# Optimization experiments

Hardware: AMD Instinct MI355X
Metric: run time of the kernel (lower is better)

## Reference

```python
import jax, jax.numpy as jnp
import numpy as np


def conv1x1(x, w, b):
    # x: [B,C,H,W], w: [O,C], b: [O]
    return jnp.einsum('bchw,oc->bohw', x, w) + b[None, :, None, None]


def dwconv(x, w):
    # depthwise conv, x: [B,C,H,W], w: [C,1,k,k], SAME padding (k odd, pad=k//2)
    return jax.lax.conv_general_dilated(
        x, w, window_strides=(1, 1), padding='SAME',
        dimension_numbers=('NCHW', 'OIHW', 'NCHW'),
        feature_group_count=x.shape[1])


def setup_inputs() -> dict:
    key = jax.random.key(0)
    ks = jax.random.split(key, 14)
    B, C, H, W = 16, 256, 64, 64
    OC = C // 16  # scale=16 -> 16
    WSCALE = 0.05
    r = lambda k, shape: jax.random.normal(k, shape, dtype=jnp.float32) * WSCALE
    return {
        'x': jax.random.normal(ks[0], (B, C, H, W), dtype=jnp.float32),
        'conv_w': r(ks[1], (C + 4, C)),           # 1x1 conv -> ctx (C) + gates (3+1)
        'conv_b': r(ks[2], (C + 4,)),
        'fw3': r(ks[3], (C, 1, 3, 3)),            # depthwise focal kernels
        'fw5': r(ks[4], (C, 1, 5, 5)),
        'fw7': r(ks[5], (C, 1, 7, 7)),
        'key_w': r(ks[6], (1, C)),                # Conv_key 1x1
        'key_b': r(ks[7], (1,)),
        'v1_w': r(ks[8], (OC, C)),                # Conv_value first 1x1
        'v1_b': r(ks[9], (OC,)),
        'ln_w': jnp.ones((OC,), dtype=jnp.float32),
        'ln_b': jnp.zeros((OC,), dtype=jnp.float32),
        'v2_w': r(ks[10], (C, OC)),               # Conv_value second 1x1
        'v2_b': r(ks[11], (C,)),
    }


def reference(x, conv_w, conv_b, fw3, fw5, fw7, key_w, key_b,
              v1_w, v1_b, ln_w, ln_b, v2_w, v2_b):
    B, C, H, W = x.shape
    # _contextAggregation
    t = conv1x1(x, conv_w, conv_b)          # [B, C+4, H, W]
    ctx, gates = t[:, :C], t[:, C:]         # [B,C,H,W], [B,4,H,W]
    ctx_all = jnp.zeros_like(ctx)
    for l, fw in enumerate((fw3, fw5, fw7)):
        ctx = jax.nn.gelu(dwconv(ctx, fw), approximate=False)  # torch GELU = exact erf
        ctx_all = ctx_all + ctx * gates[:, l:l + 1]
    ctx_global = jnp.mean(ctx, axis=(2, 3), keepdims=True)     # AdaptiveAvgPool2d(1)
    ctx_all = ctx_all + ctx_global * gates[:, 3:4]
    # GC-style channel attention: softmax over spatial positions
    k = conv1x1(ctx_all, key_w, key_b).reshape(B, H * W)       # [B, HW]
    k = jax.nn.softmax(k, axis=1)
    q = ctx_all.reshape(B, C, H * W)
    qk = jnp.einsum('bcn,bn->bc', q, k)[:, :, None, None]      # [B,C,1,1]
    # Conv_value: 1x1 -> LayerNorm([OC,1,1]) -> ReLU -> 1x1
    v = conv1x1(qk, v1_w, v1_b)                                # [B,OC,1,1]
    mu = jnp.mean(v, axis=(1, 2, 3), keepdims=True)
    var = jnp.var(v, axis=(1, 2, 3), keepdims=True)
    v = (v - mu) * jax.lax.rsqrt(var + 1e-5)
    v = v * ln_w[None, :, None, None] + ln_b[None, :, None, None]
    v = jax.nn.relu(v)
    v = conv1x1(v, v2_w, v2_b)                                 # [B,C,1,1]
    return ctx_all + v
```

## Files before the change

### kernel.cpp

```cpp
#include <hip/hip_runtime.h>

#define DEVFN __device__ __forceinline__

constexpr int B  = 16;
constexpr int C  = 256;
constexpr int N  = 64 * 64;
constexpr int O1 = C + 4;

typedef __attribute__((ext_vector_type(8)))  short bf16x8;
typedef __attribute__((ext_vector_type(4)))  short bf16x4;
typedef __attribute__((ext_vector_type(16))) float f32x16;
typedef unsigned short ushort_t;

DEVFN short f2bf(float f){
  union { float f; unsigned u; } p; p.f = f;
  unsigned r = p.u + 0x7fffu + ((p.u >> 16) & 1u);
  return (short)(r >> 16);
}
DEVFN float lo2f(unsigned u){ union{unsigned u; float f;} p; p.u = u << 16; return p.f; }
DEVFN float hi2f(unsigned u){ union{unsigned u; float f;} p; p.u = u & 0xffff0000u; return p.f; }

DEVFN float gelu_fast(float x){
  float y = 1.5957691216f * fmaf(0.044715f * x * x, x, x);
  return x / (1.0f + __expf(-y));
}

__global__ __launch_bounds__(256, 4)
void k_conv1_mfma(const float* __restrict__ x, const float* __restrict__ w,
                  const float* __restrict__ bias, ushort_t* __restrict__ ctxb,
                  float* __restrict__ gates){
  __shared__ __align__(16) short wlds[16 * 64 * 8];
  __shared__ __align__(16) short xlds[16 * 64 * 8];
  const int tid  = threadIdx.x;
  const int wv   = tid >> 6;
  const int lane = tid & 63;
  const int l31  = lane & 31;
  const int lhi  = lane >> 5;
  const int oBase = blockIdx.y * 64;
  const int pg0   = blockIdx.x * 64;
  const int b  = pg0 >> 12;
  const int n0 = pg0 & 4095;
  const int mw = (wv >> 1) * 32;
  const int nw = (wv & 1) * 32;

  f32x16 acc;
  #pragma unroll
  for(int r = 0; r < 16; r++) acc[r] = 0.f;

  const int rstage = tid & 63;
  const int kg0    = (tid >> 6) * 4;

  for(int kc = 0; kc < 256; kc += 128){
    __syncthreads();
    {
      const int o = oBase + rstage;
      const float* wp = w + o * 256 + kc;
      #pragma unroll
      for(int t = 0; t < 4; t++){
        const int kg = kg0 + t;
        bf16x8 v;
        if(o < O1){
          const float4 f0 = *(const float4*)(wp + kg * 8);
          const float4 f1 = *(const float4*)(wp + kg * 8 + 4);
          v[0] = f2bf(f0.x); v[1] = f2bf(f0.y); v[2] = f2bf(f0.z); v[3] = f2bf(f0.w);
          v[4] = f2bf(f1.x); v[5] = f2bf(f1.y); v[6] = f2bf(f1.z); v[7] = f2bf(f1.w);
        } else {
          #pragma unroll
          for(int j = 0; j < 8; j++) v[j] = 0;
        }
        *(bf16x8*)&wlds[(kg * 64 + rstage) * 8] = v;
      }
    }
    {
      const float* xp = x + (size_t)b * C * N + (size_t)kc * N + n0 + rstage;
      #pragma unroll
      for(int t = 0; t < 4; t++){
        const int kg = kg0 + t;
        float f[8];
        #pragma unroll
        for(int j = 0; j < 8; j++) f[j] = xp[(size_t)(kg * 8 + j) * N];
        bf16x8 v;
        #pragma unroll
        for(int j = 0; j < 8; j++) v[j] = f2bf(f[j]);
        *(bf16x8*)&xlds[(kg * 64 + rstage) * 8] = v;
      }
    }
    __syncthreads();
    #pragma unroll
    for(int ks = 0; ks < 8; ks++){
      const int kg = ks * 2 + lhi;
      bf16x8 af = *(const bf16x8*)&wlds[(kg * 64 + mw + l31) * 8];
      bf16x8 bfr = *(const bf16x8*)&xlds[(kg * 64 + nw + l31) * 8];
      acc = __builtin_amdgcn_mfma_f32_32x32x16_bf16(af, bfr, acc, 0, 0, 0);
    }
  }

  const int n = n0 + nw + l31;
  #pragma unroll
  for(int r = 0; r < 16; r++){
    const int row = (r & 3) + 8 * (r >> 2) + 4 * lhi;
    const int o = oBase + mw + row;
    if(o >= O1) continue;
    const float v = acc[r] + bias[o];
    if(o < 256)
      ctxb[((size_t)(b * 256 + o)) * N + n] = (ushort_t)f2bf(v);
    else
      gates[((size_t)(b * 4 + (o - 256))) * N + n] = v;
  }
}

constexpr int SSTR = 72;

DEVFN void unpack16(const short* p, float* wnd){
  uint4 a = *(const uint4*)p;
  uint4 b = *(const uint4*)(p + 8);
  unsigned ua[8] = {a.x, a.y, a.z, a.w, b.x, b.y, b.z, b.w};
  #pragma unroll
  for(int d = 0; d < 8; d++){ wnd[2*d] = lo2f(ua[d]); wnd[2*d+1] = hi2f(ua[d]); }
}

template<int K>
DEVFN void dw_stage(const short* src, const float* __restrict__ fw, int c,
                    int h, int w0, float* val){
  constexpr int R = K / 2;
  float acc[8];
  #pragma unroll
  for(int i = 0; i < 8; i++) acc[i] = 0.f;
  #pragma unroll
  for(int ky = 0; ky < K; ky++){
    const int r = h + ky - R;
    if((unsigned)r < 64u){
      float wnd[16];
      unpack16(&src[r * SSTR + w0], wnd);
      #pragma unroll
      for(int kx = 0; kx < K; kx++){
        const float wv = fw[c * K * K + ky * K + kx];
        #pragma unroll
        for(int i = 0; i < 8; i++)
          acc[i] = fmaf(wnd[i + kx + 4 - R], wv, acc[i]);
      }
    }
  }
  #pragma unroll
  for(int i = 0; i < 8; i++) val[i] = gelu_fast(acc[i]);
}

DEVFN void store_row(short* dst, int h, int w0, const float* val){
  bf16x4 lo, hi;
  #pragma unroll
  for(int i = 0; i < 4; i++){ lo[i] = f2bf(val[i]); hi[i] = f2bf(val[i + 4]); }
  *(bf16x4*)&dst[h * SSTR + w0 + 4] = lo;
  *(bf16x4*)&dst[h * SSTR + w0 + 8] = hi;
}

__global__ __launch_bounds__(512, 6)
void k_dwchain(const ushort_t* __restrict__ ctxb, const float* __restrict__ fw3,
               const float* __restrict__ fw5, const float* __restrict__ fw7,
               const float* __restrict__ gates, float* __restrict__ out){
  __shared__ __align__(16) short bufA[64 * SSTR];
  __shared__ __align__(16) short bufB[64 * SSTR];
  __shared__ float red[512];
  const int tid = threadIdx.x;
  const int plane = blockIdx.x;
  const int b = plane >> 8;
  const int c = plane & 255;
  const int h  = tid >> 3;
  const int w0 = (tid & 7) * 8;
  const int nbase = h * 64 + w0;

  if(tid < 64){
    bf16x4 z = {0, 0, 0, 0};
    *(bf16x4*)&bufA[tid * SSTR] = z;  *(bf16x4*)&bufA[tid * SSTR + 68] = z;
    *(bf16x4*)&bufB[tid * SSTR] = z;  *(bf16x4*)&bufB[tid * SSTR + 68] = z;
  }
  {
    bf16x8 iv = *(const bf16x8*)((const short*)ctxb + (size_t)plane * N + tid * 8);
    bf16x4 lo, hi;
    #pragma unroll
    for(int j = 0; j < 4; j++){ lo[j] = iv[j]; hi[j] = iv[j + 4]; }
    *(bf16x4*)&bufA[h * SSTR + w0 + 4] = lo;
    *(bf16x4*)&bufA[h * SSTR + w0 + 8] = hi;
  }
  __syncthreads();

  float ctxp[8];
  #pragma unroll
  for(int i = 0; i < 8; i++) ctxp[i] = 0.f;
  float val[8];

  dw_stage<3>(bufA, fw3, c, h, w0, val);
  {
    const float* gp = gates + ((size_t)(b * 4 + 0)) * N + nbase;
    float4 ga = *(const float4*)gp, gb = *(const float4*)(gp + 4);
    ctxp[0] = fmaf(val[0], ga.x, ctxp[0]); ctxp[1] = fmaf(val[1], ga.y, ctxp[1]);
    ctxp[2] = fmaf(val[2], ga.z, ctxp[2]); ctxp[3] = fmaf(val[3], ga.w, ctxp[3]);
    ctxp[4] = fmaf(val[4], gb.x, ctxp[4]); ctxp[5] = fmaf(val[5], gb.y, ctxp[5]);
    ctxp[6] = fmaf(val[6], gb.z, ctxp[6]); ctxp[7] = fmaf(val[7], gb.w, ctxp[7]);
    store_row(bufB, h, w0, val);
  }
  __syncthreads();

  dw_stage<5>(bufB, fw5, c, h, w0, val);
  {
    const float* gp = gates + ((size_t)(b * 4 + 1)) * N + nbase;
    float4 ga = *(const float4*)gp, gb = *(const float4*)(gp + 4);
    ctxp[0] = fmaf(val[0], ga.x, ctxp[0]); ctxp[1] = fmaf(val[1], ga.y, ctxp[1]);
    ctxp[2] = fmaf(val[2], ga.z, ctxp[2]); ctxp[3] = fmaf(val[3], ga.w, ctxp[3]);
    ctxp[4] = fmaf(val[4], gb.x, ctxp[4]); ctxp[5] = fmaf(val[5], gb.y, ctxp[5]);
    ctxp[6] = fmaf(val[6], gb.z, ctxp[6]); ctxp[7] = fmaf(val[7], gb.w, ctxp[7]);
    store_row(bufA, h, w0, val);
  }
  __syncthreads();

  dw_stage<7>(bufA, fw7, c, h, w0, val);
  float lsum = 0.f;
  {
    const float* gp = gates + ((size_t)(b * 4 + 2)) * N + nbase;
    float4 ga = *(const float4*)gp, gb = *(const float4*)(gp + 4);
    ctxp[0] = fmaf(val[0], ga.x, ctxp[0]); ctxp[1] = fmaf(val[1], ga.y, ctxp[1]);
    ctxp[2] = fmaf(val[2], ga.z, ctxp[2]); ctxp[3] = fmaf(val[3], ga.w, ctxp[3]);
    ctxp[4] = fmaf(val[4], gb.x, ctxp[4]); ctxp[5] = fmaf(val[5], gb.y, ctxp[5]);
    ctxp[6] = fmaf(val[6], gb.z, ctxp[6]); ctxp[7] = fmaf(val[7], gb.w, ctxp[7]);
    #pragma unroll
    for(int i = 0; i < 8; i++) lsum += val[i];
  }
  red[tid] = lsum;
  __syncthreads();
  for(int s = 256; s > 0; s >>= 1){
    if(tid < s) red[tid] += red[tid + s];
    __syncthreads();
  }
  const float mean = red[0] * (1.0f / 4096.0f);

  {
    const float* gp = gates + ((size_t)(b * 4 + 3)) * N + nbase;
    float4 ga = *(const float4*)gp, gb = *(const float4*)(gp + 4);
    float4 o0, o1;
    o0.x = fmaf(mean, ga.x, ctxp[0]); o0.y = fmaf(mean, ga.y, ctxp[1]);
    o0.z = fmaf(mean, ga.z, ctxp[2]); o0.w = fmaf(mean, ga.w, ctxp[3]);
    o1.x = fmaf(mean, gb.x, ctxp[4]); o1.y = fmaf(mean, gb.y, ctxp[5]);
    o1.z = fmaf(mean, gb.z, ctxp[6]); o1.w = fmaf(mean, gb.w, ctxp[7]);
    float* op = out + (size_t)plane * N + nbase;
    *(float4*)op = o0;
    *(float4*)(op + 4) = o1;
  }
}

__global__ __launch_bounds__(256)
void k_logits(const float* __restrict__ P, const float* __restrict__ key_w,
              const float* __restrict__ key_b, float* __restrict__ logits){
  __shared__ float kw[256];
  __shared__ float part[256];
  int tid = threadIdx.x;
  kw[tid] = key_w[tid];
  __syncthreads();
  int b = blockIdx.x >> 6;
  int n0 = (blockIdx.x & 63) * 64;
  int cpart = tid >> 6, px = tid & 63;
  const float* pp = P + ((size_t)(b * 256 + cpart * 64)) * N + n0 + px;
  float acc = 0.f;
  #pragma unroll 8
  for(int c = 0; c < 64; c++)
    acc = fmaf(kw[cpart * 64 + c], pp[(size_t)c * N], acc);
  part[tid] = acc;
  __syncthreads();
  if(tid < 64){
    float l = part[tid] + part[64 + tid] + part[128 + tid] + part[192 + tid];
    logits[b * N + n0 + tid] = l + key_b[0];
  }
}

__global__ __launch_bounds__(256)
void k_softmax(float* __restrict__ kbuf){
  __shared__ float red[256];
  int b = blockIdx.x, tid = threadIdx.x;
  float v[16];
  float m = -1e30f;
  #pragma unroll
  for(int i = 0; i < 16; i++){
    v[i] = kbuf[b * N + tid + i * 256];
    m = fmaxf(m, v[i]);
  }
  red[tid] = m; __syncthreads();
  for(int s = 128; s > 0; s >>= 1){
    if(tid < s) red[tid] = fmaxf(red[tid], red[tid + s]);
    __syncthreads();
  }
  m = red[0]; __syncthreads();
  float ssum = 0.f;
  #pragma unroll
  for(int i = 0; i < 16; i++){ v[i] = __expf(v[i] - m); ssum += v[i]; }
  red[tid] = ssum; __syncthreads();
  for(int s = 128; s > 0; s >>= 1){
    if(tid < s) red[tid] += red[tid + s];
    __syncthreads();
  }
  float inv = 1.0f / red[0];
  #pragma unroll
  for(int i = 0; i < 16; i++)
    kbuf[b * N + tid + i * 256] = v[i] * inv;
}

__global__ __launch_bounds__(256)
void k_qk(const float* __restrict__ P, const float* __restrict__ kbuf,
          float* __restrict__ qk){
  __shared__ float red[256];
  int plane = blockIdx.x, tid = threadIdx.x;
  int b = plane >> 8;
  const float* pp = P + (size_t)plane * N;
  const float* kp = kbuf + b * N;
  float acc = 0.f;
  #pragma unroll
  for(int i = 0; i < 16; i++){
    int n = tid + i * 256;
    acc = fmaf(pp[n], kp[n], acc);
  }
  red[tid] = acc; __syncthreads();
  for(int s = 128; s > 0; s >>= 1){
    if(tid < s) red[tid] += red[tid + s];
    __syncthreads();
  }
  if(tid == 0) qk[plane] = red[0];
}

__global__ __launch_bounds__(256)
void k_v(const float* __restrict__ qk, const float* __restrict__ v1w,
         const float* __restrict__ v1b, const float* __restrict__ lnw,
         const float* __restrict__ lnb, const float* __restrict__ v2w,
         const float* __restrict__ v2b, float* __restrict__ vout){
  int b = blockIdx.x, tid = threadIdx.x;
  __shared__ float qs[256];
  __shared__ float part[256];
  __shared__ float v1s[16];
  __shared__ float vr[16];
  __shared__ float stats[2];
  qs[tid] = qk[b * 256 + tid];
  __syncthreads();
  int oc = tid >> 4, ln = tid & 15;
  float p = 0.f;
  #pragma unroll
  for(int j = 0; j < 16; j++){
    int cc = ln + j * 16;
    p = fmaf(v1w[oc * 256 + cc], qs[cc], p);
  }
  part[tid] = p;
  __syncthreads();
  if(tid < 16){
    float s = v1b[tid];
    for(int j = 0; j < 16; j++) s += part[tid * 16 + j];
    v1s[tid] = s;
  }
  __syncthreads();
  if(tid == 0){
    float mu = 0.f;
    for(int i = 0; i < 16; i++) mu += v1s[i];
    mu *= (1.f / 16.f);
    float var = 0.f;
    for(int i = 0; i < 16; i++){ float d = v1s[i] - mu; var += d * d; }
    var *= (1.f / 16.f);
    stats[0] = mu; stats[1] = rsqrtf(var + 1e-5f);
  }
  __syncthreads();
  if(tid < 16){
    float vv = (v1s[tid] - stats[0]) * stats[1] * lnw[tid] + lnb[tid];
    vr[tid] = fmaxf(vv, 0.f);
  }
  __syncthreads();
  float o = v2b[tid];
  #pragma unroll
  for(int j = 0; j < 16; j++) o = fmaf(v2w[tid * 16 + j], vr[j], o);
  vout[b * 256 + tid] = o;
}

__global__ __launch_bounds__(256)
void k_final(float* __restrict__ out, const float* __restrict__ vout){
  int idx = blockIdx.x * 256 + threadIdx.x;
  int plane = idx >> 10;
  float4 p = *((float4*)out + idx);
  float vv = vout[plane];
  p.x += vv; p.y += vv; p.z += vv; p.w += vv;
  *((float4*)out + idx) = p;
}

extern "C" void kernel_launch(void* const* d_in, const int* in_sizes, int n_in,
                              void* d_out, int out_size, void* d_ws, size_t ws_size,
                              hipStream_t stream){
  const float* x      = (const float*)d_in[0];
  const float* conv_w = (const float*)d_in[1];
  const float* conv_b = (const float*)d_in[2];
  const float* fw3    = (const float*)d_in[3];
  const float* fw5    = (const float*)d_in[4];
  const float* fw7    = (const float*)d_in[5];
  const float* key_w  = (const float*)d_in[6];
  const float* key_b  = (const float*)d_in[7];
  const float* v1_w   = (const float*)d_in[8];
  const float* v1_b   = (const float*)d_in[9];
  const float* ln_w   = (const float*)d_in[10];
  const float* ln_b   = (const float*)d_in[11];
  const float* v2_w   = (const float*)d_in[12];
  const float* v2_b   = (const float*)d_in[13];
  float* out = (float*)d_out;

  const size_t PL = (size_t)B * C * N;
  char* p = (char*)d_ws;
  ushort_t* ctxb = (ushort_t*)p;  p += PL * sizeof(ushort_t);
  float* gates   = (float*)p;     p += (size_t)B * 4 * N * sizeof(float);
  float* kbuf    = (float*)p;     p += (size_t)B * N * sizeof(float);
  float* qkb     = (float*)p;     p += (size_t)B * C * sizeof(float);
  float* vout    = (float*)p;

  k_conv1_mfma<<<dim3(1024, 5), 256, 0, stream>>>(x, conv_w, conv_b, ctxb, gates);
  k_dwchain<<<B * C, 512, 0, stream>>>(ctxb, fw3, fw5, fw7, gates, out);
  k_logits<<<1024, 256, 0, stream>>>(out, key_w, key_b, kbuf);
  k_softmax<<<B, 256, 0, stream>>>(kbuf);
  k_qk<<<B * C, 256, 0, stream>>>(out, kbuf, qkb);
  k_v<<<B, 256, 0, stream>>>(qkb, v1_w, v1_b, ln_w, ln_b, v2_w, v2_b, vout);
  k_final<<<16384, 256, 0, stream>>>(out, vout);
}
```

Before: 312.3 us.

## Store ctx_all as bf16 in place and keep dwconv LDS tiles in fp32

The depthwise chain now writes ctx_all as bf16 back into the ctxb buffer instead of fp32 to out, so k_logits, k_qk and k_final each read half the bytes. k_final expands bf16 to fp32 and adds the value vector. Inside k_dwchain the LDS tiles become fp32, which removes per-tap bf16 unpacking but doubles shared memory. The block reduction switches to wave shuffles, GELU uses a reciprocal instruction, and launch bounds are raised to 8. Rounding ctx_all to bf16 adds error to the final output.

```diff
diff --git a/kernel.cpp b/kernel.cpp
--- a/kernel.cpp
+++ b/kernel.cpp
@@ -19,10 +19,12 @@
 }
 DEVFN float lo2f(unsigned u){ union{unsigned u; float f;} p; p.u = u << 16; return p.f; }
 DEVFN float hi2f(unsigned u){ union{unsigned u; float f;} p; p.u = u & 0xffff0000u; return p.f; }
+DEVFN float bf2f(ushort_t s){ union{unsigned u; float f;} p; p.u = (unsigned)s << 16; return p.f; }
 
 DEVFN float gelu_fast(float x){
   float y = 1.5957691216f * fmaf(0.044715f * x * x, x, x);
-  return x / (1.0f + __expf(-y));
+  float s = __builtin_amdgcn_rcpf(1.0f + __expf(-y));
+  return x * s;
 }
 
 __global__ __launch_bounds__(256, 4)
@@ -109,18 +111,10 @@
   }
 }
 
-constexpr int SSTR = 72;
-
-DEVFN void unpack16(const short* p, float* wnd){
-  uint4 a = *(const uint4*)p;
-  uint4 b = *(const uint4*)(p + 8);
-  unsigned ua[8] = {a.x, a.y, a.z, a.w, b.x, b.y, b.z, b.w};
-  #pragma unroll
-  for(int d = 0; d < 8; d++){ wnd[2*d] = lo2f(ua[d]); wnd[2*d+1] = hi2f(ua[d]); }
-}
+constexpr int FSTR = 72;
 
 template<int K>
-DEVFN void dw_stage(const short* src, const float* __restrict__ fw, int c,
+DEVFN void dw_stage(const float* src, const float* __restrict__ fw, int c,
                     int h, int w0, float* val){
   constexpr int R = K / 2;
   float acc[8];
@@ -130,8 +124,13 @@
   for(int ky = 0; ky < K; ky++){
     const int r = h + ky - R;
     if((unsigned)r < 64u){
+      const float* rp = &src[r * FSTR + w0];
       float wnd[16];
-      unpack16(&src[r * SSTR + w0], wnd);
+      #pragma unroll
+      for(int q = 0; q < 4; q++){
+        float4 v4 = *(const float4*)(rp + q * 4);
+        wnd[q*4+0] = v4.x; wnd[q*4+1] = v4.y; wnd[q*4+2] = v4.z; wnd[q*4+3] = v4.w;
+      }
       #pragma unroll
       for(int kx = 0; kx < K; kx++){
         const float wv = fw[c * K * K + ky * K + kx];
@@ -145,21 +144,21 @@
   for(int i = 0; i < 8; i++) val[i] = gelu_fast(acc[i]);
 }
 
-DEVFN void store_row(short* dst, int h, int w0, const float* val){
-  bf16x4 lo, hi;
-  #pragma unroll
-  for(int i = 0; i < 4; i++){ lo[i] = f2bf(val[i]); hi[i] = f2bf(val[i + 4]); }
-  *(bf16x4*)&dst[h * SSTR + w0 + 4] = lo;
-  *(bf16x4*)&dst[h * SSTR + w0 + 8] = hi;
-}
-
-__global__ __launch_bounds__(512, 6)
-void k_dwchain(const ushort_t* __restrict__ ctxb, const float* __restrict__ fw3,
+DEVFN void store_row(float* dst, int h, int w0, const float* val){
+  float4 a, b;
+  a.x = val[0]; a.y = val[1]; a.z = val[2]; a.w = val[3];
+  b.x = val[4]; b.y = val[5]; b.z = val[6]; b.w = val[7];
+  *(float4*)&dst[h * FSTR + w0 + 4] = a;
+  *(float4*)&dst[h * FSTR + w0 + 8] = b;
+}
+
+__global__ __launch_bounds__(512, 8)
+void k_dwchain(ushort_t* __restrict__ ctxb, const float* __restrict__ fw3,
                const float* __restrict__ fw5, const float* __restrict__ fw7,
-               const float* __restrict__ gates, float* __restrict__ out){
-  __shared__ __align__(16) short bufA[64 * SSTR];
-  __shared__ __align__(16) short bufB[64 * SSTR];
-  __shared__ float red[512];
+               const float* __restrict__ gates){
+  __shared__ __align__(16) float bufA[64 * FSTR];
+  __shared__ __align__(16) float bufB[64 * FSTR];
+  __shared__ float wred[8];
   const int tid = threadIdx.x;
   const int plane = blockIdx.x;
   const int b = plane >> 8;
@@ -169,17 +168,19 @@
   const int nbase = h * 64 + w0;
 
   if(tid < 64){
-    bf16x4 z = {0, 0, 0, 0};
-    *(bf16x4*)&bufA[tid * SSTR] = z;  *(bf16x4*)&bufA[tid * SSTR + 68] = z;
-    *(bf16x4*)&bufB[tid * SSTR] = z;  *(bf16x4*)&bufB[tid * SSTR + 68] = z;
+    float4 z = {0.f, 0.f, 0.f, 0.f};
+    *(float4*)&bufA[tid * FSTR] = z;  *(float4*)&bufA[tid * FSTR + 68] = z;
+    *(float4*)&bufB[tid * FSTR] = z;  *(float4*)&bufB[tid * FSTR + 68] = z;
   }
   {
     bf16x8 iv = *(const bf16x8*)((const short*)ctxb + (size_t)plane * N + tid * 8);
-    bf16x4 lo, hi;
-    #pragma unroll
-    for(int j = 0; j < 4; j++){ lo[j] = iv[j]; hi[j] = iv[j + 4]; }
-    *(bf16x4*)&bufA[h * SSTR + w0 + 4] = lo;
-    *(bf16x4*)&bufA[h * SSTR + w0 + 8] = hi;
+    float4 a, bq;
+    a.x  = bf2f((ushort_t)iv[0]); a.y  = bf2f((ushort_t)iv[1]);
+    a.z  = bf2f((ushort_t)iv[2]); a.w  = bf2f((ushort_t)iv[3]);
+    bq.x = bf2f((ushort_t)iv[4]); bq.y = bf2f((ushort_t)iv[5]);
+    bq.z = bf2f((ushort_t)iv[6]); bq.w = bf2f((ushort_t)iv[7]);
+    *(float4*)&bufA[h * FSTR + w0 + 4] = a;
+    *(float4*)&bufA[h * FSTR + w0 + 8] = bq;
   }
   __syncthreads();
 
@@ -224,48 +225,52 @@
     #pragma unroll
     for(int i = 0; i < 8; i++) lsum += val[i];
   }
-  red[tid] = lsum;
-  __syncthreads();
-  for(int s = 256; s > 0; s >>= 1){
-    if(tid < s) red[tid] += red[tid + s];
-    __syncthreads();
-  }
-  const float mean = red[0] * (1.0f / 4096.0f);
+  #pragma unroll
+  for(int off = 32; off > 0; off >>= 1) lsum += __shfl_xor(lsum, off, 64);
+  if((tid & 63) == 0) wred[tid >> 6] = lsum;
+  __syncthreads();
+  float mean = 0.f;
+  #pragma unroll
+  for(int i = 0; i < 8; i++) mean += wred[i];
+  mean *= (1.0f / 4096.0f);
 
   {
     const float* gp = gates + ((size_t)(b * 4 + 3)) * N + nbase;
     float4 ga = *(const float4*)gp, gb = *(const float4*)(gp + 4);
-    float4 o0, o1;
-    o0.x = fmaf(mean, ga.x, ctxp[0]); o0.y = fmaf(mean, ga.y, ctxp[1]);
-    o0.z = fmaf(mean, ga.z, ctxp[2]); o0.w = fmaf(mean, ga.w, ctxp[3]);
-    o1.x = fmaf(mean, gb.x, ctxp[4]); o1.y = fmaf(mean, gb.y, ctxp[5]);
-    o1.z = fmaf(mean, gb.z, ctxp[6]); o1.w = fmaf(mean, gb.w, ctxp[7]);
-    float* op = out + (size_t)plane * N + nbase;
-    *(float4*)op = o0;
-    *(float4*)(op + 4) = o1;
+    bf16x8 ov;
+    ov[0] = f2bf(fmaf(mean, ga.x, ctxp[0])); ov[1] = f2bf(fmaf(mean, ga.y, ctxp[1]));
+    ov[2] = f2bf(fmaf(mean, ga.z, ctxp[2])); ov[3] = f2bf(fmaf(mean, ga.w, ctxp[3]));
+    ov[4] = f2bf(fmaf(mean, gb.x, ctxp[4])); ov[5] = f2bf(fmaf(mean, gb.y, ctxp[5]));
+    ov[6] = f2bf(fmaf(mean, gb.z, ctxp[6])); ov[7] = f2bf(fmaf(mean, gb.w, ctxp[7]));
+    *(bf16x8*)((short*)ctxb + (size_t)plane * N + nbase) = ov;
   }
 }
 
 __global__ __launch_bounds__(256)
-void k_logits(const float* __restrict__ P, const float* __restrict__ key_w,
+void k_logits(const ushort_t* __restrict__ P, const float* __restrict__ key_w,
               const float* __restrict__ key_b, float* __restrict__ logits){
   __shared__ float kw[256];
-  __shared__ float part[256];
+  __shared__ float part[512];
   int tid = threadIdx.x;
   kw[tid] = key_w[tid];
   __syncthreads();
-  int b = blockIdx.x >> 6;
-  int n0 = (blockIdx.x & 63) * 64;
-  int cpart = tid >> 6, px = tid & 63;
-  const float* pp = P + ((size_t)(b * 256 + cpart * 64)) * N + n0 + px;
-  float acc = 0.f;
+  int b  = blockIdx.x >> 5;
+  int n0 = (blockIdx.x & 31) * 128;
+  int cpart = tid >> 6, pxp = tid & 63;
+  const ushort_t* pp = P + ((size_t)(b * 256 + cpart * 64)) * N + n0 + pxp * 2;
+  float a0 = 0.f, a1 = 0.f;
   #pragma unroll 8
-  for(int c = 0; c < 64; c++)
-    acc = fmaf(kw[cpart * 64 + c], pp[(size_t)c * N], acc);
-  part[tid] = acc;
-  __syncthreads();
-  if(tid < 64){
-    float l = part[tid] + part[64 + tid] + part[128 + tid] + part[192 + tid];
+  for(int c = 0; c < 64; c++){
+    unsigned u = *(const unsigned*)(pp + (size_t)c * N);
+    float kwv = kw[cpart * 64 + c];
+    a0 = fmaf(lo2f(u), kwv, a0);
+    a1 = fmaf(hi2f(u), kwv, a1);
+  }
+  part[cpart * 128 + pxp * 2]     = a0;
+  part[cpart * 128 + pxp * 2 + 1] = a1;
+  __syncthreads();
+  if(tid < 128){
+    float l = part[tid] + part[128 + tid] + part[256 + tid] + part[384 + tid];
     logits[b * N + n0 + tid] = l + key_b[0];
   }
 }
@@ -302,18 +307,21 @@
 }
 
 __global__ __launch_bounds__(256)
-void k_qk(const float* __restrict__ P, const float* __restrict__ kbuf,
+void k_qk(const ushort_t* __restrict__ P, const float* __restrict__ kbuf,
           float* __restrict__ qk){
   __shared__ float red[256];
   int plane = blockIdx.x, tid = threadIdx.x;
   int b = plane >> 8;
-  const float* pp = P + (size_t)plane * N;
-  const float* kp = kbuf + b * N;
+  const unsigned* pp = (const unsigned*)(P + (size_t)plane * N);
+  const float2* kp = (const float2*)(kbuf + b * N);
   float acc = 0.f;
   #pragma unroll
-  for(int i = 0; i < 16; i++){
-    int n = tid + i * 256;
-    acc = fmaf(pp[n], kp[n], acc);
+  for(int i = 0; i < 8; i++){
+    int idx = tid + i * 256;
+    unsigned u = pp[idx];
+    float2 kk = kp[idx];
+    acc = fmaf(lo2f(u), kk.x, acc);
+    acc = fmaf(hi2f(u), kk.y, acc);
   }
   red[tid] = acc; __syncthreads();
   for(int s = 128; s > 0; s >>= 1){
@@ -373,13 +381,21 @@
 }
 
 __global__ __launch_bounds__(256)
-void k_final(float* __restrict__ out, const float* __restrict__ vout){
-  int idx = blockIdx.x * 256 + threadIdx.x;
-  int plane = idx >> 10;
-  float4 p = *((float4*)out + idx);
+void k_final(float* __restrict__ out, const ushort_t* __restrict__ ctxb,
+             const float* __restrict__ vout){
+  int idx8 = blockIdx.x * 256 + threadIdx.x;
+  int plane = idx8 >> 9;
+  int off = (idx8 & 511) * 8;
+  bf16x8 v = *(const bf16x8*)((const short*)ctxb + (size_t)plane * N + off);
   float vv = vout[plane];
-  p.x += vv; p.y += vv; p.z += vv; p.w += vv;
-  *((float4*)out + idx) = p;
+  float4 o0, o1;
+  o0.x = bf2f((ushort_t)v[0]) + vv; o0.y = bf2f((ushort_t)v[1]) + vv;
+  o0.z = bf2f((ushort_t)v[2]) + vv; o0.w = bf2f((ushort_t)v[3]) + vv;
+  o1.x = bf2f((ushort_t)v[4]) + vv; o1.y = bf2f((ushort_t)v[5]) + vv;
+  o1.z = bf2f((ushort_t)v[6]) + vv; o1.w = bf2f((ushort_t)v[7]) + vv;
+  float* op = out + (size_t)plane * N + off;
+  *(float4*)op = o0;
+  *(float4*)(op + 4) = o1;
 }
 
 extern "C" void kernel_launch(void* const* d_in, const int* in_sizes, int n_in,
@@ -410,10 +426,10 @@
   float* vout    = (float*)p;
 
   k_conv1_mfma<<<dim3(1024, 5), 256, 0, stream>>>(x, conv_w, conv_b, ctxb, gates);
-  k_dwchain<<<B * C, 512, 0, stream>>>(ctxb, fw3, fw5, fw7, gates, out);
-  k_logits<<<1024, 256, 0, stream>>>(out, key_w, key_b, kbuf);
+  k_dwchain<<<B * C, 512, 0, stream>>>(ctxb, fw3, fw5, fw7, gates);
+  k_logits<<<512, 256, 0, stream>>>(ctxb, key_w, key_b, kbuf);
   k_softmax<<<B, 256, 0, stream>>>(kbuf);
-  k_qk<<<B * C, 256, 0, stream>>>(out, kbuf, qkb);
+  k_qk<<<B * C, 256, 0, stream>>>(ctxb, kbuf, qkb);
   k_v<<<B, 256, 0, stream>>>(qkb, v1_w, v1_b, ln_w, ln_b, v2_w, v2_b, vout);
-  k_final<<<16384, 256, 0, stream>>>(out, vout);
-}
+  k_final<<<8192, 256, 0, stream>>>(out, ctxb, vout);
+}
```

New measurement: 401.7 us. 28.6% more time.
